# Kernel tuning notes

Measured on AMD Instinct MI355X. Metric: run time of the kernel, lower is better.

Reference implementation:

```python
import jax, jax.numpy as jnp
import numpy as np

NEG_INF = -1e30


def setup_inputs() -> dict:
    key = jax.random.key(0)
    k1, k2, k3 = jax.random.split(key, 3)
    B, H, HKV, S, D = 2, 16, 4, 2048, 128
    q = jax.random.normal(k1, (B, H, S, D), dtype=jnp.float32)
    k = jax.random.normal(k2, (B, HKV, S, D), dtype=jnp.float32)
    v = jax.random.normal(k3, (B, HKV, S, D), dtype=jnp.float32)
    return {"q": q, "k": k, "v": v}


def reference(q, k, v):
    # Flash attention math (exact, non-tiled reference): causal + sliding-window
    # masked softmax(QK^T * scale) V with GQA head grouping.
    B, H, M, D = q.shape
    _, HKV, N, _ = k.shape
    G = H // HKV  # num_kv_groups
    W = 512       # sliding window size
    scale = 1.0 / jnp.sqrt(jnp.float32(D))

    qg = q.reshape(B, HKV, G, M, D)
    # scores: [B, HKV, G, M, N]
    scores = jnp.einsum("bkgmd,bknd->bkgmn", qg, k) * scale

    i = jnp.arange(M)[:, None]
    j = jnp.arange(N)[None, :]
    # causal: j <= i ; sliding window: only last W keys visible (i - j < W)
    keep = (j <= i) & ((i - j) < W)
    scores = jnp.where(keep[None, None, None], scores, NEG_INF)

    p = jax.nn.softmax(scores.astype(jnp.float32), axis=-1).astype(q.dtype)
    out = jnp.einsum("bkgmn,bknd->bkgmd", p, v)
    return out.reshape(B, H, M, D)
```

## Files before the change

kernel.cpp:

```cpp
#include <hip/hip_runtime.h>
#include <hip/hip_bf16.h>
#include <stdint.h>

#define SEQ 2048
#define HD  128
#define WIN 512
#define NH  16
#define NKV 4
#define BATCH 2

typedef __attribute__((ext_vector_type(8))) short bf16x8;
typedef __attribute__((ext_vector_type(4))) float f32x4;

#define EXP2(x) __builtin_amdgcn_exp2f(x)

#define KSTR 136
#define VSTR 72
#define PSTR 72

__device__ __forceinline__ uint32_t pk2(float a, float b) {
    __hip_bfloat162 h = __float22bfloat162_rn(make_float2(a, b));
    return *reinterpret_cast<uint32_t*>(&h);
}
__device__ __forceinline__ uint16_t pk1(float a) {
    __hip_bfloat16 h = __float2bfloat16(a);
    return *reinterpret_cast<uint16_t*>(&h);
}

__global__ __launch_bounds__(256, 2) void fa_mfma(
    const float* __restrict__ q,
    const float* __restrict__ k,
    const float* __restrict__ v,
    float* __restrict__ out)
{
    const int tid  = threadIdx.x;
    const int wave = tid >> 6;
    const int lane = tid & 63;
    const int l4   = lane >> 4;
    const int l15  = lane & 15;

    const int bh   = blockIdx.x >> 4;
    const int qblk = blockIdx.x & 15;
    const int q0   = qblk << 7;
    const int hkv  = (bh & (NH - 1)) >> 2;
    const int b    = bh >> 4;

    const int i0   = q0 + wave * 32;

    __shared__ __align__(16) uint16_t lds_k[64 * KSTR];
    __shared__ __align__(16) uint16_t lds_vt[HD * VSTR];
    __shared__ __align__(16) uint16_t lds_p[4 * 32 * PSTR];
    uint16_t* pw = &lds_p[wave * 32 * PSTR];

    const float scale2 = 0.08838834764831845f * 1.4426950408889634f;

    const size_t qbase  = (size_t)bh * SEQ * HD;
    const size_t kvbase = (size_t)(b * NKV + hkv) * SEQ * HD;

    union { bf16x8 f; uint32_t u[4]; } qf[2][4];
    #pragma unroll
    for (int nt = 0; nt < 2; ++nt) {
        const float* qr = q + qbase + (size_t)(i0 + nt * 16 + l15) * HD;
        #pragma unroll
        for (int ks = 0; ks < 4; ++ks) {
            const float4* g = reinterpret_cast<const float4*>(qr + ks * 32 + l4 * 8);
            float4 a = g[0], bq = g[1];
            qf[nt][ks].u[0] = pk2(a.x * scale2, a.y * scale2);
            qf[nt][ks].u[1] = pk2(a.z * scale2, a.w * scale2);
            qf[nt][ks].u[2] = pk2(bq.x * scale2, bq.y * scale2);
            qf[nt][ks].u[3] = pk2(bq.z * scale2, bq.w * scale2);
        }
    }

    f32x4 O[2][8];
    #pragma unroll
    for (int a1 = 0; a1 < 2; ++a1)
        #pragma unroll
        for (int a2 = 0; a2 < 8; ++a2) O[a1][a2] = (f32x4){0.f, 0.f, 0.f, 0.f};
    float mrow[2] = {-1e30f, -1e30f};
    float lrow[2] = {0.f, 0.f};

    const int kt_lo_blk = (q0 >= 512) ? ((q0 - 511) >> 6) : 0;
    const int kt_hi_blk = (q0 + 127) >> 6;
    const int lo_w = (i0 >= 512) ? ((i0 - 511) >> 6) : 0;
    const int hi_w = (i0 + 31) >> 6;

    const int vdg = tid & 31;
    const int vkg = tid >> 5;
    float4 rKa[4], rKb[4], rV[8];

    auto prefetch = [&](int kt) {
        const float* kp = k + kvbase + (size_t)kt * 64 * HD;
        const float* vp = v + kvbase + (size_t)kt * 64 * HD;
        #pragma unroll
        for (int it = 0; it < 4; ++it) {
            int flat8 = tid + it * 256, key = flat8 >> 4, ch = flat8 & 15;
            const float4* g = reinterpret_cast<const float4*>(kp + key * HD + ch * 8);
            rKa[it] = g[0]; rKb[it] = g[1];
        }
        #pragma unroll
        for (int r = 0; r < 8; ++r)
            rV[r] = *reinterpret_cast<const float4*>(vp + (vkg * 8 + r) * HD + vdg * 4);
    };

    prefetch(kt_lo_blk);

    for (int kt = kt_lo_blk; kt <= kt_hi_blk; ++kt) {
        #pragma unroll
        for (int it = 0; it < 4; ++it) {
            int flat8 = tid + it * 256, key = flat8 >> 4, ch = flat8 & 15;
            uint4 wv;
            wv.x = pk2(rKa[it].x, rKa[it].y);  wv.y = pk2(rKa[it].z, rKa[it].w);
            wv.z = pk2(rKb[it].x, rKb[it].y);  wv.w = pk2(rKb[it].z, rKb[it].w);
            *reinterpret_cast<uint4*>(&lds_k[key * KSTR + ch * 8]) = wv;
        }
        {
            const float* rvf = reinterpret_cast<const float*>(rV);
            #pragma unroll
            for (int i = 0; i < 4; ++i) {
                uint4 wv;
                wv.x = pk2(rvf[0 * 4 + i], rvf[1 * 4 + i]);
                wv.y = pk2(rvf[2 * 4 + i], rvf[3 * 4 + i]);
                wv.z = pk2(rvf[4 * 4 + i], rvf[5 * 4 + i]);
                wv.w = pk2(rvf[6 * 4 + i], rvf[7 * 4 + i]);
                *reinterpret_cast<uint4*>(&lds_vt[(vdg * 4 + i) * VSTR + vkg * 8]) = wv;
            }
        }
        __syncthreads();

        if (kt < kt_hi_blk) prefetch(kt + 1);

        if (kt >= lo_w && kt <= hi_w) {
            f32x4 sf[4][2];
            #pragma unroll
            for (int mt = 0; mt < 4; ++mt) {
                #pragma unroll
                for (int nt = 0; nt < 2; ++nt) sf[mt][nt] = (f32x4){0.f, 0.f, 0.f, 0.f};
                #pragma unroll
                for (int ks = 0; ks < 4; ++ks) {
                    bf16x8 af = *reinterpret_cast<const bf16x8*>(
                        &lds_k[(mt * 16 + l15) * KSTR + ks * 32 + l4 * 8]);
                    #pragma unroll
                    for (int nt = 0; nt < 2; ++nt)
                        sf[mt][nt] = __builtin_amdgcn_mfma_f32_16x16x32_bf16(
                            af, qf[nt][ks].f, sf[mt][nt], 0, 0, 0);
                }
            }
            const bool needmask = (kt == hi_w) || (kt == lo_w && i0 > 511);
            if (needmask) {
                #pragma unroll
                for (int mt = 0; mt < 4; ++mt) {
                    int jb = kt * 64 + mt * 16 + l4 * 4;
                    #pragma unroll
                    for (int nt = 0; nt < 2; ++nt) {
                        int iq = i0 + nt * 16 + l15;
                        #pragma unroll
                        for (int r = 0; r < 4; ++r) {
                            int j = jb + r;
                            if (!((j <= iq) && (iq - j < WIN))) sf[mt][nt][r] = -1e30f;
                        }
                    }
                }
            }
            float alpha[2];
            #pragma unroll
            for (int nt = 0; nt < 2; ++nt) {
                float tm = -1e30f;
                #pragma unroll
                for (int mt = 0; mt < 4; ++mt)
                    #pragma unroll
                    for (int r = 0; r < 4; ++r) tm = fmaxf(tm, sf[mt][nt][r]);
                tm = fmaxf(tm, __shfl_xor(tm, 16, 64));
                tm = fmaxf(tm, __shfl_xor(tm, 32, 64));
                float mn = fmaxf(mrow[nt], tm);
                alpha[nt] = EXP2(mrow[nt] - mn);
                mrow[nt] = mn;
                float me = fmaxf(mn, -1e20f);
                float ts = 0.f;
                #pragma unroll
                for (int mt = 0; mt < 4; ++mt) {
                    #pragma unroll
                    for (int r = 0; r < 4; ++r) {
                        float pv = EXP2(sf[mt][nt][r] - me);
                        ts += pv;
                        pw[(nt * 16 + l15) * PSTR + mt * 16 + l4 * 4 + r] = pk1(pv);
                    }
                }
                ts += __shfl_xor(ts, 16, 64);
                ts += __shfl_xor(ts, 32, 64);
                lrow[nt] = lrow[nt] * alpha[nt] + ts;
            }
            #pragma unroll
            for (int mt = 0; mt < 2; ++mt) {
                #pragma unroll
                for (int r = 0; r < 4; ++r) {
                    float ar = __shfl(alpha[mt], l4 * 4 + r, 64);
                    #pragma unroll
                    for (int nt = 0; nt < 8; ++nt) O[mt][nt][r] *= ar;
                }
            }
            #pragma unroll
            for (int ks = 0; ks < 2; ++ks) {
                bf16x8 pa[2];
                #pragma unroll
                for (int mt = 0; mt < 2; ++mt)
                    pa[mt] = *reinterpret_cast<const bf16x8*>(
                        &pw[(mt * 16 + l15) * PSTR + ks * 32 + l4 * 8]);
                #pragma unroll
                for (int nt = 0; nt < 8; ++nt) {
                    bf16x8 vf = *reinterpret_cast<const bf16x8*>(
                        &lds_vt[(nt * 16 + l15) * VSTR + ks * 32 + l4 * 8]);
                    #pragma unroll
                    for (int mt = 0; mt < 2; ++mt)
                        O[mt][nt] = __builtin_amdgcn_mfma_f32_16x16x32_bf16(
                            pa[mt], vf, O[mt][nt], 0, 0, 0);
                }
            }
        }
        __syncthreads();
    }

    #pragma unroll
    for (int mt = 0; mt < 2; ++mt) {
        float inv = 1.0f / lrow[mt];
        #pragma unroll
        for (int r = 0; r < 4; ++r) {
            float li = __shfl(inv, l4 * 4 + r, 64);
            int row = i0 + mt * 16 + l4 * 4 + r;
            float* orow = out + qbase + (size_t)row * HD;
            #pragma unroll
            for (int nt = 0; nt < 8; ++nt)
                orow[nt * 16 + l15] = O[mt][nt][r] * li;
        }
    }
}

extern "C" void kernel_launch(void* const* d_in, const int* in_sizes, int n_in,
                              void* d_out, int out_size, void* d_ws, size_t ws_size,
                              hipStream_t stream) {
    const float* q = (const float*)d_in[0];
    const float* k = (const float*)d_in[1];
    const float* v = (const float*)d_in[2];
    float* out     = (float*)d_out;

    hipLaunchKernelGGL(fa_mfma, dim3(BATCH * NH * (SEQ / 128)), dim3(256), 0, stream,
                       q, k, v, out);
}
```

Before: 130.4 us.

## Keep P in registers via transposed PV MFMA and halve query tile

The query tile per block shrinks from 128 to 64 rows (16 per wave), doubling the grid and raising the occupancy target to 4 blocks per CU. The PV product is transposed so O^T accumulates with the 16x16x16 bf16 MFMA, taking P directly from the QK^T accumulator registers. This removes the P round-trip through LDS, the per-row alpha shuffles and the scalar output stores, which now become float4 writes. The cost is that K/V tiles are loaded and converted to bf16 twice as often per query row, and a smaller MFMA shape is used for PV.

```diff
diff --git a/kernel.cpp b/kernel.cpp
--- a/kernel.cpp
+++ b/kernel.cpp
@@ -10,24 +10,20 @@
 #define BATCH 2
 
 typedef __attribute__((ext_vector_type(8))) short bf16x8;
+typedef __attribute__((ext_vector_type(4))) short bf16x4;
 typedef __attribute__((ext_vector_type(4))) float f32x4;
 
 #define EXP2(x) __builtin_amdgcn_exp2f(x)
 
 #define KSTR 136
 #define VSTR 72
-#define PSTR 72
 
 __device__ __forceinline__ uint32_t pk2(float a, float b) {
     __hip_bfloat162 h = __float22bfloat162_rn(make_float2(a, b));
     return *reinterpret_cast<uint32_t*>(&h);
 }
-__device__ __forceinline__ uint16_t pk1(float a) {
-    __hip_bfloat16 h = __float2bfloat16(a);
-    return *reinterpret_cast<uint16_t*>(&h);
-}
-
-__global__ __launch_bounds__(256, 2) void fa_mfma(
+
+__global__ __launch_bounds__(256, 4) void fa_mfma2(
     const float* __restrict__ q,
     const float* __restrict__ k,
     const float* __restrict__ v,
@@ -39,51 +35,45 @@
     const int l4   = lane >> 4;
     const int l15  = lane & 15;
 
-    const int bh   = blockIdx.x >> 4;
-    const int qblk = blockIdx.x & 15;
-    const int q0   = qblk << 7;
+    const int bh   = blockIdx.x >> 5;
+    const int qblk = blockIdx.x & 31;
+    const int q0   = qblk << 6;
     const int hkv  = (bh & (NH - 1)) >> 2;
     const int b    = bh >> 4;
 
-    const int i0   = q0 + wave * 32;
+    const int i0   = q0 + wave * 16;
 
     __shared__ __align__(16) uint16_t lds_k[64 * KSTR];
     __shared__ __align__(16) uint16_t lds_vt[HD * VSTR];
-    __shared__ __align__(16) uint16_t lds_p[4 * 32 * PSTR];
-    uint16_t* pw = &lds_p[wave * 32 * PSTR];
 
     const float scale2 = 0.08838834764831845f * 1.4426950408889634f;
 
     const size_t qbase  = (size_t)bh * SEQ * HD;
     const size_t kvbase = (size_t)(b * NKV + hkv) * SEQ * HD;
 
-    union { bf16x8 f; uint32_t u[4]; } qf[2][4];
-    #pragma unroll
-    for (int nt = 0; nt < 2; ++nt) {
-        const float* qr = q + qbase + (size_t)(i0 + nt * 16 + l15) * HD;
+    union { bf16x8 f; uint32_t u[4]; } qf[4];
+    {
+        const float* qr = q + qbase + (size_t)(i0 + l15) * HD;
         #pragma unroll
         for (int ks = 0; ks < 4; ++ks) {
             const float4* g = reinterpret_cast<const float4*>(qr + ks * 32 + l4 * 8);
             float4 a = g[0], bq = g[1];
-            qf[nt][ks].u[0] = pk2(a.x * scale2, a.y * scale2);
-            qf[nt][ks].u[1] = pk2(a.z * scale2, a.w * scale2);
-            qf[nt][ks].u[2] = pk2(bq.x * scale2, bq.y * scale2);
-            qf[nt][ks].u[3] = pk2(bq.z * scale2, bq.w * scale2);
+            qf[ks].u[0] = pk2(a.x * scale2, a.y * scale2);
+            qf[ks].u[1] = pk2(a.z * scale2, a.w * scale2);
+            qf[ks].u[2] = pk2(bq.x * scale2, bq.y * scale2);
+            qf[ks].u[3] = pk2(bq.z * scale2, bq.w * scale2);
         }
     }
 
-    f32x4 O[2][8];
+    f32x4 O[8];
     #pragma unroll
-    for (int a1 = 0; a1 < 2; ++a1)
-        #pragma unroll
-        for (int a2 = 0; a2 < 8; ++a2) O[a1][a2] = (f32x4){0.f, 0.f, 0.f, 0.f};
-    float mrow[2] = {-1e30f, -1e30f};
-    float lrow[2] = {0.f, 0.f};
+    for (int a2 = 0; a2 < 8; ++a2) O[a2] = (f32x4){0.f, 0.f, 0.f, 0.f};
+    float mrow = -1e30f, lrow = 0.f;
 
     const int kt_lo_blk = (q0 >= 512) ? ((q0 - 511) >> 6) : 0;
-    const int kt_hi_blk = (q0 + 127) >> 6;
+    const int kt_hi_blk = (q0 + 63) >> 6;
     const int lo_w = (i0 >= 512) ? ((i0 - 511) >> 6) : 0;
-    const int hi_w = (i0 + 31) >> 6;
+    const int hi_w = (i0 + 15) >> 6;
 
     const int vdg = tid & 31;
     const int vkg = tid >> 5;
@@ -131,107 +121,80 @@
         if (kt < kt_hi_blk) prefetch(kt + 1);
 
         if (kt >= lo_w && kt <= hi_w) {
-            f32x4 sf[4][2];
+            f32x4 sf[4];
             #pragma unroll
             for (int mt = 0; mt < 4; ++mt) {
-                #pragma unroll
-                for (int nt = 0; nt < 2; ++nt) sf[mt][nt] = (f32x4){0.f, 0.f, 0.f, 0.f};
+                sf[mt] = (f32x4){0.f, 0.f, 0.f, 0.f};
                 #pragma unroll
                 for (int ks = 0; ks < 4; ++ks) {
                     bf16x8 af = *reinterpret_cast<const bf16x8*>(
                         &lds_k[(mt * 16 + l15) * KSTR + ks * 32 + l4 * 8]);
-                    #pragma unroll
-                    for (int nt = 0; nt < 2; ++nt)
-                        sf[mt][nt] = __builtin_amdgcn_mfma_f32_16x16x32_bf16(
-                            af, qf[nt][ks].f, sf[mt][nt], 0, 0, 0);
+                    sf[mt] = __builtin_amdgcn_mfma_f32_16x16x32_bf16(
+                        af, qf[ks].f, sf[mt], 0, 0, 0);
                 }
             }
             const bool needmask = (kt == hi_w) || (kt == lo_w && i0 > 511);
             if (needmask) {
+                const int iq = i0 + l15;
                 #pragma unroll
                 for (int mt = 0; mt < 4; ++mt) {
                     int jb = kt * 64 + mt * 16 + l4 * 4;
                     #pragma unroll
-                    for (int nt = 0; nt < 2; ++nt) {
-                        int iq = i0 + nt * 16 + l15;
-                        #pragma unroll
-                        for (int r = 0; r < 4; ++r) {
-                            int j = jb + r;
-                            if (!((j <= iq) && (iq - j < WIN))) sf[mt][nt][r] = -1e30f;
-                        }
+                    for (int r = 0; r < 4; ++r) {
+                        int j = jb + r;
+                        if (!((j <= iq) && (iq - j < WIN))) sf[mt][r] = -1e30f;
                     }
                 }
             }
-            float alpha[2];
-            #pragma unroll
-            for (int nt = 0; nt < 2; ++nt) {
-                float tm = -1e30f;
-                #pragma unroll
-                for (int mt = 0; mt < 4; ++mt)
-                    #pragma unroll
-                    for (int r = 0; r < 4; ++r) tm = fmaxf(tm, sf[mt][nt][r]);
-                tm = fmaxf(tm, __shfl_xor(tm, 16, 64));
-                tm = fmaxf(tm, __shfl_xor(tm, 32, 64));
-                float mn = fmaxf(mrow[nt], tm);
-                alpha[nt] = EXP2(mrow[nt] - mn);
-                mrow[nt] = mn;
-                float me = fmaxf(mn, -1e20f);
-                float ts = 0.f;
-                #pragma unroll
-                for (int mt = 0; mt < 4; ++mt) {
-                    #pragma unroll
-                    for (int r = 0; r < 4; ++r) {
-                        float pv = EXP2(sf[mt][nt][r] - me);
-                        ts += pv;
-                        pw[(nt * 16 + l15) * PSTR + mt * 16 + l4 * 4 + r] = pk1(pv);
-                    }
-                }
-                ts += __shfl_xor(ts, 16, 64);
-                ts += __shfl_xor(ts, 32, 64);
-                lrow[nt] = lrow[nt] * alpha[nt] + ts;
-            }
-            #pragma unroll
-            for (int mt = 0; mt < 2; ++mt) {
-                #pragma unroll
-                for (int r = 0; r < 4; ++r) {
-                    float ar = __shfl(alpha[mt], l4 * 4 + r, 64);
-                    #pragma unroll
-                    for (int nt = 0; nt < 8; ++nt) O[mt][nt][r] *= ar;
-                }
-            }
-            #pragma unroll
-            for (int ks = 0; ks < 2; ++ks) {
-                bf16x8 pa[2];
-                #pragma unroll
-                for (int mt = 0; mt < 2; ++mt)
-                    pa[mt] = *reinterpret_cast<const bf16x8*>(
-                        &pw[(mt * 16 + l15) * PSTR + ks * 32 + l4 * 8]);
-                #pragma unroll
-                for (int nt = 0; nt < 8; ++nt) {
-                    bf16x8 vf = *reinterpret_cast<const bf16x8*>(
-                        &lds_vt[(nt * 16 + l15) * VSTR + ks * 32 + l4 * 8]);
-                    #pragma unroll
-                    for (int mt = 0; mt < 2; ++mt)
-                        O[mt][nt] = __builtin_amdgcn_mfma_f32_16x16x32_bf16(
-                            pa[mt], vf, O[mt][nt], 0, 0, 0);
+            float tm = -1e30f;
+            #pragma unroll
+            for (int mt = 0; mt < 4; ++mt)
+                #pragma unroll
+                for (int r = 0; r < 4; ++r) tm = fmaxf(tm, sf[mt][r]);
+            tm = fmaxf(tm, __shfl_xor(tm, 16, 64));
+            tm = fmaxf(tm, __shfl_xor(tm, 32, 64));
+            float mn    = fmaxf(mrow, tm);
+            float alpha = EXP2(mrow - mn);
+            mrow = mn;
+            float me = fmaxf(mn, -1e20f);
+            union { bf16x4 v; uint32_t u[2]; } pb[4];
+            float ts = 0.f;
+            #pragma unroll
+            for (int mt = 0; mt < 4; ++mt) {
+                float p0 = EXP2(sf[mt][0] - me), p1 = EXP2(sf[mt][1] - me);
+                float p2 = EXP2(sf[mt][2] - me), p3 = EXP2(sf[mt][3] - me);
+                ts += (p0 + p1) + (p2 + p3);
+                pb[mt].u[0] = pk2(p0, p1);
+                pb[mt].u[1] = pk2(p2, p3);
+            }
+            ts += __shfl_xor(ts, 16, 64);
+            ts += __shfl_xor(ts, 32, 64);
+            lrow = lrow * alpha + ts;
+            #pragma unroll
+            for (int mtd = 0; mtd < 8; ++mtd)
+                #pragma unroll
+                for (int r = 0; r < 4; ++r) O[mtd][r] *= alpha;
+            #pragma unroll
+            for (int ks = 0; ks < 4; ++ks) {
+                #pragma unroll
+                for (int mtd = 0; mtd < 8; ++mtd) {
+                    bf16x4 vf = *reinterpret_cast<const bf16x4*>(
+                        &lds_vt[(mtd * 16 + l15) * VSTR + ks * 16 + l4 * 4]);
+                    O[mtd] = __builtin_amdgcn_mfma_f32_16x16x16bf16_1k(
+                        vf, pb[ks].v, O[mtd], 0, 0, 0);
                 }
             }
         }
         __syncthreads();
     }
 
+    const float inv = 1.0f / lrow;
+    float* orow = out + qbase + (size_t)(i0 + l15) * HD + l4 * 4;
     #pragma unroll
-    for (int mt = 0; mt < 2; ++mt) {
-        float inv = 1.0f / lrow[mt];
-        #pragma unroll
-        for (int r = 0; r < 4; ++r) {
-            float li = __shfl(inv, l4 * 4 + r, 64);
-            int row = i0 + mt * 16 + l4 * 4 + r;
-            float* orow = out + qbase + (size_t)row * HD;
-            #pragma unroll
-            for (int nt = 0; nt < 8; ++nt)
-                orow[nt * 16 + l15] = O[mt][nt][r] * li;
-        }
+    for (int mtd = 0; mtd < 8; ++mtd) {
+        float4 st = make_float4(O[mtd][0] * inv, O[mtd][1] * inv,
+                                O[mtd][2] * inv, O[mtd][3] * inv);
+        *reinterpret_cast<float4*>(orow + mtd * 16) = st;
     }
 }
 
@@ -243,6 +206,6 @@
     const float* v = (const float*)d_in[2];
     float* out     = (float*)d_out;
 
-    hipLaunchKernelGGL(fa_mfma, dim3(BATCH * NH * (SEQ / 128)), dim3(256), 0, stream,
+    hipLaunchKernelGGL(fa_mfma2, dim3(BATCH * NH * (SEQ / 64)), dim3(256), 0, stream,
                        q, k, v, out);
 }
```

Result: slower. 269.5 us (+106.7%).
